# Optimization experiments

Measured on AMD Instinct MI355X. Metric: run time of the kernel, lower is better.

Reference implementation:

```python
import jax, jax.numpy as jnp
import numpy as np

N_RES = 8192
N_IN = 128
BATCH = 16
RES_NNZ = int(0.1 * N_RES * N_RES)  # 6710886
IN_NNZ = int(0.1 * N_RES * N_IN)    # 104857
LEAK = 0.9


def spmm_coo(vals, rows, cols, inputs, n_out):
    """COO SpMM: out[b, r] = sum_{n: rows[n]==r} vals[n] * inputs[b, cols[n]].
    Equivalent to (coo_matmat(vals, rows, cols, inputs.T, shape=(n_out, F)).T)."""
    contrib = vals[:, None] * inputs.T[cols]  # [nnz, B]
    return jax.ops.segment_sum(contrib, rows, num_segments=n_out).T  # [B, n_out]


def leaky_erf(z, state, a=LEAK):
    return (1.0 - a) * state + a * jax.scipy.special.erf(z)


def setup_inputs() -> dict:
    key = jax.random.key(0)
    ks = jax.random.split(key, 10)
    return {
        "state": jax.random.normal(ks[0], (BATCH, N_RES), jnp.float32),
        "x": jax.random.normal(ks[1], (BATCH, N_IN), jnp.float32),
        "res_vals": jax.random.normal(ks[2], (RES_NNZ,), jnp.float32),
        "res_rows": jax.random.randint(ks[3], (RES_NNZ,), 0, N_RES, jnp.int32),
        "res_cols": jax.random.randint(ks[4], (RES_NNZ,), 0, N_RES, jnp.int32),
        "res_bias": jax.random.normal(ks[5], (N_RES,), jnp.float32),
        "in_vals": jax.random.normal(ks[6], (IN_NNZ,), jnp.float32),
        "in_rows": jax.random.randint(ks[7], (IN_NNZ,), 0, N_RES, jnp.int32),
        "in_cols": jax.random.randint(ks[8], (IN_NNZ,), 0, N_IN, jnp.int32),
        "in_bias": jax.random.normal(ks[9], (N_RES,), jnp.float32),
    }


def reference(state, x, res_vals, res_rows, res_cols, res_bias,
              in_vals, in_rows, in_cols, in_bias):
    z_res = spmm_coo(res_vals, res_rows, res_cols, state, N_RES) + res_bias
    z_in = spmm_coo(in_vals, in_rows, in_cols, x, N_RES) + in_bias
    return leaky_erf(z_in + z_res, state)
```

## Files before the change

kernel.cpp:

```cpp
#include <hip/hip_runtime.h>
#include <math.h>

#define N_RES 8192
#define N_IN  128
#define BATCH 16
#define LEAK  0.9f

#define NBK   256
#define CAP1B 28672
#define CHUNK 4096
#define SB2   (CAP1B / CHUNK)
#define TBLK  128


#define OFF_SRCT 0
#define OFF_BCUR (1u << 20)
#define OFF_PART (2u << 20)
#define OFF_E1   (8u << 20)
#define REQ_A    ((size_t)OFF_E1 + (size_t)NBK * CAP1B * 8)

__global__ __launch_bounds__(256) void pass1_fused(
    const float* __restrict__ state,
    const float* __restrict__ x,
    const float* __restrict__ vres, const int* __restrict__ rres,
    const int* __restrict__ cres, int nres, int nbres,
    const float* __restrict__ vin, const int* __restrict__ rin,
    const int* __restrict__ cin, int nin, int nchunks,
    float* __restrict__ srcT,
    uint2* __restrict__ e1,
    int* __restrict__ bcur) {
  int tid = threadIdx.x;

  if (blockIdx.x >= nchunks) {
    int idx0 = (blockIdx.x - nchunks) * 256 + tid;
    const int stride = TBLK * 256;
    for (int i = idx0; i < N_RES * BATCH; i += stride) {
      int b = i >> 13;
      int r = i & (N_RES - 1);
      srcT[r * BATCH + b] = state[i];
    }
    for (int i = idx0; i < N_IN * BATCH; i += stride) {
      int b = i >> 7;
      int c = i & (N_IN - 1);
      srcT[(N_RES + c) * BATCH + b] = x[i];
    }
    return;
  }

  const float* vals; const int* rows; const int* cols;
  int nnz, col_off, base;
  if (blockIdx.x < nbres) {
    vals = vres; rows = rres; cols = cres; nnz = nres; col_off = 0;
    base = blockIdx.x * CHUNK;
  } else {
    vals = vin; rows = rin; cols = cin; nnz = nin; col_off = N_RES;
    base = (blockIdx.x - nbres) * CHUNK;
  }

  __shared__ uint2 stg[CHUNK];
  __shared__ int hist[NBK];
  __shared__ int lbase[NBK];
  __shared__ int gbase[NBK];
  __shared__ int wsum[4];
  int wave = tid >> 6, lane = tid & 63;

  hist[tid] = 0;
  __syncthreads();

  int n = nnz - base;
  if (n > CHUNK) n = CHUNK;

  uint2 ent[16];
  int bb[16], lp[16];
#pragma unroll
  for (int e = 0; e < 16; ++e) {
    int i = e * 256 + tid;
    bb[e] = -1;
    if (i < n) {
      int r = rows[base + i];
      int c = cols[base + i] + col_off;
      float v = vals[base + i];
      bb[e] = r >> 5;
      ent[e] = make_uint2(__float_as_uint(v),
                          ((unsigned)r << 14) | (unsigned)c);
      lp[e] = atomicAdd(&hist[bb[e]], 1);
    }
  }
  __syncthreads();
  int h = hist[tid];
  int v = h;
#pragma unroll
  for (int d = 1; d < 64; d <<= 1) {
    int t = __shfl_up(v, d);
    if (lane >= d) v += t;
  }
  if (lane == 63) wsum[wave] = v;
  __syncthreads();
  int off = 0;
#pragma unroll
  for (int w = 0; w < 4; ++w)
    if (w < wave) off += wsum[w];
  lbase[tid] = off + v - h;
  gbase[tid] = h ? atomicAdd(&bcur[tid], h) : 0;
  __syncthreads();
#pragma unroll
  for (int e = 0; e < 16; ++e) {
    if (bb[e] >= 0) stg[lbase[bb[e]] + lp[e]] = ent[e];
  }
  __syncthreads();
  for (int i = tid; i < n; i += 256) {
    uint2 ld = stg[i];
    int b = (int)(ld.y >> 19);
    int p = gbase[b] + (i - lbase[b]);
    if (p < CAP1B) e1[(size_t)b * CAP1B + p] = ld;
  }
}

__global__ __launch_bounds__(256) void pass2_accum(
    const uint2* __restrict__ e1,
    const int* __restrict__ bcur,
    const float* __restrict__ srcT,
    float* __restrict__ partials) {
  int bucket = blockIdx.x / SB2;
  int ch = blockIdx.x - bucket * SB2;
  int tid = threadIdx.x;
  float* __restrict__ pb = partials + (size_t)blockIdx.x * 512;

  int cnt = bcur[bucket];
  if (cnt > CAP1B) cnt = CAP1B;
  int base = ch * CHUNK;
  if (base >= cnt) {
    for (int i = tid; i < 512; i += 256) pb[i] = 0.0f;
    return;
  }
  int n = cnt - base;
  if (n > CHUNK) n = CHUNK;

  __shared__ uint2 stg[CHUNK];
  __shared__ int hist[32];
  __shared__ int sbase[33];
  if (tid < 32) hist[tid] = 0;
  __syncthreads();

  const uint2* __restrict__ src = e1 + (size_t)bucket * CAP1B + base;
  uint2 ent[16];
  int rr_[16], lp[16];
#pragma unroll
  for (int e = 0; e < 16; ++e) {
    int i = e * 256 + tid;
    rr_[e] = -1;
    if (i < n) {
      ent[e] = src[i];
      rr_[e] = (int)((ent[e].y >> 14) & 31u);
      lp[e] = atomicAdd(&hist[rr_[e]], 1);
    }
  }
  __syncthreads();
  if (tid < 64) {
    int hh = (tid < 32) ? hist[tid] : 0;
    int vv = hh;
#pragma unroll
    for (int d = 1; d < 32; d <<= 1) {
      int t = __shfl_up(vv, d);
      if ((tid & 63) >= d) vv += t;
    }
    if (tid < 32) sbase[tid] = vv - hh;
    if (tid == 31) sbase[32] = vv;
  }
  __syncthreads();
#pragma unroll
  for (int e = 0; e < 16; ++e)
    if (rr_[e] >= 0) stg[sbase[rr_[e]] + lp[e]] = ent[e];
  __syncthreads();

  int wave = tid >> 6, lane = tid & 63;
  int q = lane >> 4;
  int sub = (lane >> 2) & 3;
  int bq = lane & 3;
  const float4* __restrict__ s4 = (const float4*)srcT;

  for (int rr = wave * 8; rr < wave * 8 + 8; ++rr) {
    int s0 = sbase[rr], s1 = sbase[rr + 1];
    float4 acc = make_float4(0.f, 0.f, 0.f, 0.f);
    int eoff = q * 4 + sub;
    for (int i0 = s0; i0 < s1; i0 += 16) {
      int e = i0 + eoff;
      if (e < s1) {
        uint2 ee = stg[e];
        float vv = __uint_as_float(ee.x);
        int c = (int)(ee.y & 16383u);
        float4 s = s4[c * 4 + bq];
        acc.x += vv * s.x;
        acc.y += vv * s.y;
        acc.z += vv * s.z;
        acc.w += vv * s.w;
      }
    }
#pragma unroll
    for (int m = 4; m <= 32; m <<= 1) {
      acc.x += __shfl_xor(acc.x, m);
      acc.y += __shfl_xor(acc.y, m);
      acc.z += __shfl_xor(acc.z, m);
      acc.w += __shfl_xor(acc.w, m);
    }
    if (lane < 4)
      ((float4*)(pb + rr * 16))[lane] = acc;
  }
}

__global__ __launch_bounds__(256) void finalize_fused(
    const float* __restrict__ partials,
    const float* __restrict__ state,
    const float* __restrict__ res_bias,
    const float* __restrict__ in_bias,
    float* __restrict__ out) {
  int tid = blockIdx.x * 256 + threadIdx.x;
  if (tid >= N_RES * BATCH) return;
  int b = tid >> 13;
  int r = tid & (N_RES - 1);
  int bucket = r >> 5, rr = r & 31;
  const float* __restrict__ p =
      partials + (size_t)bucket * SB2 * 512 + rr * 16 + b;
  float z = 0.0f;
#pragma unroll
  for (int ch = 0; ch < SB2; ++ch) z += p[ch * 512];
  z += res_bias[r] + in_bias[r];
  out[tid] = (1.0f - LEAK) * state[tid] + LEAK * erff(z);
}

__global__ __launch_bounds__(256) void transpose_nb(
    const float* __restrict__ state, const float* __restrict__ x,
    float* __restrict__ srcT) {
  int tid = blockIdx.x * 256 + threadIdx.x;
  if (tid < N_RES * BATCH) {
    int b = tid >> 13;
    int r = tid & (N_RES - 1);
    srcT[r * BATCH + b] = state[tid];
  }
  if (tid < N_IN * BATCH) {
    int b = tid >> 7;
    int c = tid & (N_IN - 1);
    srcT[(N_RES + c) * BATCH + b] = x[tid];
  }
}

__global__ __launch_bounds__(256) void spmm_atomic(
    const float* __restrict__ vals, const int* __restrict__ rows,
    const int* __restrict__ cols, const float* __restrict__ srcT,
    int col_off, float* __restrict__ zz, int nnz) {
  int i = blockIdx.x * blockDim.x + threadIdx.x;
  if (i >= nnz) return;
  float v = vals[i];
  int r = rows[i];
  int c = cols[i] + col_off;
  const float4* __restrict__ sp = (const float4*)(srcT + c * BATCH);
  float* zr = zz + r * BATCH;
#pragma unroll
  for (int qq = 0; qq < 4; ++qq) {
    float4 s = sp[qq];
    unsafeAtomicAdd(zr + qq * 4 + 0, v * s.x);
    unsafeAtomicAdd(zr + qq * 4 + 1, v * s.y);
    unsafeAtomicAdd(zr + qq * 4 + 2, v * s.z);
    unsafeAtomicAdd(zr + qq * 4 + 3, v * s.w);
  }
}

__global__ __launch_bounds__(256) void finalize_z(
    const float* __restrict__ z, const float* __restrict__ state,
    const float* __restrict__ res_bias, const float* __restrict__ in_bias,
    float* __restrict__ out) {
  int tid = blockIdx.x * 256 + threadIdx.x;
  if (tid >= BATCH * N_RES) return;
  int b = tid >> 13;
  int r = tid & (N_RES - 1);
  float zz = z[r * 16 + b] + res_bias[r] + in_bias[r];
  out[tid] = (1.0f - LEAK) * state[tid] + LEAK * erff(zz);
}

extern "C" void kernel_launch(void* const* d_in, const int* in_sizes, int n_in,
                              void* d_out, int out_size, void* d_ws, size_t ws_size,
                              hipStream_t stream) {
  const float* state    = (const float*)d_in[0];
  const float* x        = (const float*)d_in[1];
  const float* res_vals = (const float*)d_in[2];
  const int*   res_rows = (const int*)d_in[3];
  const int*   res_cols = (const int*)d_in[4];
  const float* res_bias = (const float*)d_in[5];
  const float* in_vals  = (const float*)d_in[6];
  const int*   in_rows  = (const int*)d_in[7];
  const int*   in_cols  = (const int*)d_in[8];
  const float* in_bias  = (const float*)d_in[9];

  const int res_nnz = in_sizes[2];
  const int in_nnz  = in_sizes[6];

  char* ws = (char*)d_ws;
  float* srcT = (float*)(ws + OFF_SRCT);
  float* out = (float*)d_out;

  if (ws_size >= REQ_A) {
    int* bcur = (int*)(ws + OFF_BCUR);
    float* partials = (float*)(ws + OFF_PART);
    uint2* e1 = (uint2*)(ws + OFF_E1);
    int nbres = (res_nnz + CHUNK - 1) / CHUNK;
    int nbin  = (in_nnz + CHUNK - 1) / CHUNK;
    int nchunks = nbres + nbin;

    hipMemsetAsync(bcur, 0, NBK * sizeof(int), stream);

    pass1_fused<<<nchunks + TBLK, 256, 0, stream>>>(
        state, x, res_vals, res_rows, res_cols, res_nnz, nbres,
        in_vals, in_rows, in_cols, in_nnz, nchunks, srcT, e1, bcur);

    pass2_accum<<<NBK * SB2, 256, 0, stream>>>(e1, bcur, srcT, partials);

    finalize_fused<<<512, 256, 0, stream>>>(
        partials, state, res_bias, in_bias, out);
  } else {
    float* z = (float*)(ws + OFF_PART);
    hipMemsetAsync(z, 0, N_RES * BATCH * sizeof(float), stream);
    transpose_nb<<<512, 256, 0, stream>>>(state, x, srcT);
    spmm_atomic<<<(res_nnz + 255) / 256, 256, 0, stream>>>(
        res_vals, res_rows, res_cols, srcT, 0, z, res_nnz);
    spmm_atomic<<<(in_nnz + 255) / 256, 256, 0, stream>>>(
        in_vals, in_rows, in_cols, srcT, N_RES, z, in_nnz);
    finalize_z<<<512, 256, 0, stream>>>(z, state, res_bias, in_bias, out);
  }
}
```

Before: 226.2 us.

## Coarsen buckets and replace pass2 row sort with LDS atomic accumulation

Bucket count drops to 128 (64 rows each) with larger per-bucket capacity, and pass1 uses smaller chunks with vectorized int4/float4 loads of the COO arrays. Pass2 no longer sorts entries by row within a chunk. It streams entries with software prefetching and accumulates into a padded shared-memory tile using LDS float atomics, then writes transposed partials that finalize reads coalesced. This removes the second histogram/scatter stage but adds shared-atomic contention. Occupancy hints are added to both kernels.

```diff
diff --git a/kernel.cpp b/kernel.cpp
--- a/kernel.cpp
+++ b/kernel.cpp
@@ -6,11 +6,12 @@
 #define BATCH 16
 #define LEAK  0.9f
 
-#define NBK   256
-#define CAP1B 28672
-#define CHUNK 4096
-#define SB2   (CAP1B / CHUNK)
-#define TBLK  128
+#define NBK    128
+#define CAP1B  55296
+#define CHUNK1 2048
+#define CHUNK2 6912
+#define SB2    8
+#define TBLK   128
 
 
 #define OFF_SRCT 0
@@ -19,7 +20,7 @@
 #define OFF_E1   (8u << 20)
 #define REQ_A    ((size_t)OFF_E1 + (size_t)NBK * CAP1B * 8)
 
-__global__ __launch_bounds__(256) void pass1_fused(
+__global__ __launch_bounds__(256, 8) void pass1_fused(
     const float* __restrict__ state,
     const float* __restrict__ x,
     const float* __restrict__ vres, const int* __restrict__ rres,
@@ -51,160 +52,148 @@
   int nnz, col_off, base;
   if (blockIdx.x < nbres) {
     vals = vres; rows = rres; cols = cres; nnz = nres; col_off = 0;
-    base = blockIdx.x * CHUNK;
+    base = blockIdx.x * CHUNK1;
   } else {
     vals = vin; rows = rin; cols = cin; nnz = nin; col_off = N_RES;
-    base = (blockIdx.x - nbres) * CHUNK;
-  }
-
-  __shared__ uint2 stg[CHUNK];
+    base = (blockIdx.x - nbres) * CHUNK1;
+  }
+
+  __shared__ uint2 stg[CHUNK1];
   __shared__ int hist[NBK];
   __shared__ int lbase[NBK];
   __shared__ int gbase[NBK];
-  __shared__ int wsum[4];
+  __shared__ int wsum[2];
   int wave = tid >> 6, lane = tid & 63;
 
-  hist[tid] = 0;
+  if (tid < NBK) hist[tid] = 0;
   __syncthreads();
 
   int n = nnz - base;
-  if (n > CHUNK) n = CHUNK;
-
-  uint2 ent[16];
-  int bb[16], lp[16];
-#pragma unroll
-  for (int e = 0; e < 16; ++e) {
-    int i = e * 256 + tid;
-    bb[e] = -1;
-    if (i < n) {
-      int r = rows[base + i];
-      int c = cols[base + i] + col_off;
-      float v = vals[base + i];
-      bb[e] = r >> 5;
-      ent[e] = make_uint2(__float_as_uint(v),
-                          ((unsigned)r << 14) | (unsigned)c);
-      lp[e] = atomicAdd(&hist[bb[e]], 1);
-    }
-  }
-  __syncthreads();
-  int h = hist[tid];
-  int v = h;
-#pragma unroll
-  for (int d = 1; d < 64; d <<= 1) {
-    int t = __shfl_up(v, d);
-    if (lane >= d) v += t;
-  }
-  if (lane == 63) wsum[wave] = v;
-  __syncthreads();
-  int off = 0;
-#pragma unroll
-  for (int w = 0; w < 4; ++w)
-    if (w < wave) off += wsum[w];
-  lbase[tid] = off + v - h;
-  gbase[tid] = h ? atomicAdd(&bcur[tid], h) : 0;
-  __syncthreads();
-#pragma unroll
-  for (int e = 0; e < 16; ++e) {
-    if (bb[e] >= 0) stg[lbase[bb[e]] + lp[e]] = ent[e];
+  if (n > CHUNK1) n = CHUNK1;
+
+  uint2 ent[8];
+  int lp[8];
+  unsigned msk = 0;
+#pragma unroll
+  for (int g = 0; g < 2; ++g) {
+    int i0 = (g * 256 + tid) * 4;
+    if (i0 + 3 < n) {
+      int4 r4 = *(const int4*)(rows + base + i0);
+      int4 c4 = *(const int4*)(cols + base + i0);
+      float4 v4 = *(const float4*)(vals + base + i0);
+      int rr_[4] = {r4.x, r4.y, r4.z, r4.w};
+      int cc_[4] = {c4.x, c4.y, c4.z, c4.w};
+      float vv_[4] = {v4.x, v4.y, v4.z, v4.w};
+#pragma unroll
+      for (int j = 0; j < 4; ++j) {
+        int e = g * 4 + j;
+        ent[e] = make_uint2(__float_as_uint(vv_[j]),
+                            ((unsigned)rr_[j] << 14) |
+                                (unsigned)(cc_[j] + col_off));
+        msk |= 1u << e;
+        lp[e] = atomicAdd(&hist[rr_[j] >> 6], 1);
+      }
+    } else {
+#pragma unroll
+      for (int j = 0; j < 4; ++j) {
+        int e = g * 4 + j, i = i0 + j;
+        if (i < n) {
+          int r = rows[base + i];
+          int c = cols[base + i] + col_off;
+          float v = vals[base + i];
+          ent[e] = make_uint2(__float_as_uint(v),
+                              ((unsigned)r << 14) | (unsigned)c);
+          msk |= 1u << e;
+          lp[e] = atomicAdd(&hist[r >> 6], 1);
+        }
+      }
+    }
+  }
+  __syncthreads();
+
+  int h = 0, v = 0;
+  if (tid < NBK) {
+    h = hist[tid];
+    v = h;
+#pragma unroll
+    for (int d = 1; d < 64; d <<= 1) {
+      int t = __shfl_up(v, d);
+      if (lane >= d) v += t;
+    }
+    if (lane == 63) wsum[wave] = v;
+  }
+  __syncthreads();
+  if (tid < NBK) {
+    int off = (wave == 1) ? wsum[0] : 0;
+    lbase[tid] = off + v - h;
+    gbase[tid] = h ? atomicAdd(&bcur[tid], h) : 0;
+  }
+  __syncthreads();
+#pragma unroll
+  for (int e = 0; e < 8; ++e) {
+    if (msk & (1u << e)) {
+      int b = (int)(ent[e].y >> 20);
+      stg[lbase[b] + lp[e]] = ent[e];
+    }
   }
   __syncthreads();
   for (int i = tid; i < n; i += 256) {
     uint2 ld = stg[i];
-    int b = (int)(ld.y >> 19);
+    int b = (int)(ld.y >> 20);
     int p = gbase[b] + (i - lbase[b]);
     if (p < CAP1B) e1[(size_t)b * CAP1B + p] = ld;
   }
 }
 
-__global__ __launch_bounds__(256) void pass2_accum(
+__global__ __launch_bounds__(256, 8) void pass2_accum(
     const uint2* __restrict__ e1,
     const int* __restrict__ bcur,
     const float* __restrict__ srcT,
     float* __restrict__ partials) {
-  int bucket = blockIdx.x / SB2;
-  int ch = blockIdx.x - bucket * SB2;
+  int bucket = blockIdx.x >> 3;
+  int ch = blockIdx.x & (SB2 - 1);
   int tid = threadIdx.x;
-  float* __restrict__ pb = partials + (size_t)blockIdx.x * 512;
+  float* __restrict__ pb = partials + (size_t)blockIdx.x * (64 * BATCH);
+
+  __shared__ float acc[64 * 17];
+  for (int i = tid; i < 64 * 17; i += 256) acc[i] = 0.0f;
 
   int cnt = bcur[bucket];
   if (cnt > CAP1B) cnt = CAP1B;
-  int base = ch * CHUNK;
-  if (base >= cnt) {
-    for (int i = tid; i < 512; i += 256) pb[i] = 0.0f;
-    return;
-  }
+  int base = ch * CHUNK2;
   int n = cnt - base;
-  if (n > CHUNK) n = CHUNK;
-
-  __shared__ uint2 stg[CHUNK];
-  __shared__ int hist[32];
-  __shared__ int sbase[33];
-  if (tid < 32) hist[tid] = 0;
+  if (n < 0) n = 0;
+  if (n > CHUNK2) n = CHUNK2;
   __syncthreads();
 
   const uint2* __restrict__ src = e1 + (size_t)bucket * CAP1B + base;
-  uint2 ent[16];
-  int rr_[16], lp[16];
-#pragma unroll
-  for (int e = 0; e < 16; ++e) {
-    int i = e * 256 + tid;
-    rr_[e] = -1;
-    if (i < n) {
-      ent[e] = src[i];
-      rr_[e] = (int)((ent[e].y >> 14) & 31u);
-      lp[e] = atomicAdd(&hist[rr_[e]], 1);
-    }
-  }
-  __syncthreads();
-  if (tid < 64) {
-    int hh = (tid < 32) ? hist[tid] : 0;
-    int vv = hh;
-#pragma unroll
-    for (int d = 1; d < 32; d <<= 1) {
-      int t = __shfl_up(vv, d);
-      if ((tid & 63) >= d) vv += t;
-    }
-    if (tid < 32) sbase[tid] = vv - hh;
-    if (tid == 31) sbase[32] = vv;
-  }
-  __syncthreads();
-#pragma unroll
-  for (int e = 0; e < 16; ++e)
-    if (rr_[e] >= 0) stg[sbase[rr_[e]] + lp[e]] = ent[e];
-  __syncthreads();
-
   int wave = tid >> 6, lane = tid & 63;
-  int q = lane >> 4;
-  int sub = (lane >> 2) & 3;
+  int sub = lane >> 2;
   int bq = lane & 3;
   const float4* __restrict__ s4 = (const float4*)srcT;
 
-  for (int rr = wave * 8; rr < wave * 8 + 8; ++rr) {
-    int s0 = sbase[rr], s1 = sbase[rr + 1];
-    float4 acc = make_float4(0.f, 0.f, 0.f, 0.f);
-    int eoff = q * 4 + sub;
-    for (int i0 = s0; i0 < s1; i0 += 16) {
-      int e = i0 + eoff;
-      if (e < s1) {
-        uint2 ee = stg[e];
-        float vv = __uint_as_float(ee.x);
-        int c = (int)(ee.y & 16383u);
-        float4 s = s4[c * 4 + bq];
-        acc.x += vv * s.x;
-        acc.y += vv * s.y;
-        acc.z += vv * s.z;
-        acc.w += vv * s.w;
-      }
-    }
-#pragma unroll
-    for (int m = 4; m <= 32; m <<= 1) {
-      acc.x += __shfl_xor(acc.x, m);
-      acc.y += __shfl_xor(acc.y, m);
-      acc.z += __shfl_xor(acc.z, m);
-      acc.w += __shfl_xor(acc.w, m);
-    }
-    if (lane < 4)
-      ((float4*)(pb + rr * 16))[lane] = acc;
+  int eI = wave * 16 + sub;
+  uint2 eeA = (eI < n) ? src[eI] : make_uint2(0u, 0u);
+  uint2 eeB = (eI + 64 < n) ? src[eI + 64] : make_uint2(0u, 0u);
+  float4 sA = s4[(int)(eeA.y & 16383u) * 4 + bq];
+  for (int i0 = wave * 16; i0 < n; i0 += 64) {
+    int e2 = i0 + 128 + sub;
+    uint2 eeC = (e2 < n) ? src[e2] : make_uint2(0u, 0u);
+    float4 sB = s4[(int)(eeB.y & 16383u) * 4 + bq];
+    float vv = __uint_as_float(eeA.x);
+    int a = (int)((eeA.y >> 14) & 63u) * 17 + (bq << 2);
+    atomicAdd(&acc[a + 0], vv * sA.x);
+    atomicAdd(&acc[a + 1], vv * sA.y);
+    atomicAdd(&acc[a + 2], vv * sA.z);
+    atomicAdd(&acc[a + 3], vv * sA.w);
+    eeA = eeB;
+    eeB = eeC;
+    sA = sB;
+  }
+  __syncthreads();
+  for (int i = tid; i < 64 * BATCH; i += 256) {
+    int b = i >> 6, rr = i & 63;
+    pb[i] = acc[rr * 17 + b];
   }
 }
 
@@ -218,12 +207,12 @@
   if (tid >= N_RES * BATCH) return;
   int b = tid >> 13;
   int r = tid & (N_RES - 1);
-  int bucket = r >> 5, rr = r & 31;
+  int bucket = r >> 6, rr = r & 63;
   const float* __restrict__ p =
-      partials + (size_t)bucket * SB2 * 512 + rr * 16 + b;
+      partials + (size_t)bucket * SB2 * (64 * BATCH) + b * 64 + rr;
   float z = 0.0f;
 #pragma unroll
-  for (int ch = 0; ch < SB2; ++ch) z += p[ch * 512];
+  for (int ch = 0; ch < SB2; ++ch) z += p[ch * (64 * BATCH)];
   z += res_bias[r] + in_bias[r];
   out[tid] = (1.0f - LEAK) * state[tid] + LEAK * erff(z);
 }
@@ -302,8 +291,8 @@
     int* bcur = (int*)(ws + OFF_BCUR);
     float* partials = (float*)(ws + OFF_PART);
     uint2* e1 = (uint2*)(ws + OFF_E1);
-    int nbres = (res_nnz + CHUNK - 1) / CHUNK;
-    int nbin  = (in_nnz + CHUNK - 1) / CHUNK;
+    int nbres = (res_nnz + CHUNK1 - 1) / CHUNK1;
+    int nbin  = (in_nnz + CHUNK1 - 1) / CHUNK1;
     int nchunks = nbres + nbin;
 
     hipMemsetAsync(bcur, 0, NBK * sizeof(int), stream);
```

Measured after the change: 740.8 us. +227.5%, slower.
